# Kernel tuning notes

Hardware: AMD Instinct MI355X
Metric: run time of the kernel (lower is better)

Reference implementation:

```python
import jax, jax.numpy as jnp
import numpy as np

D = 768
B, T = 4, 4096


def _layernorm(x, gamma, bias):
    # Faithful to the (buggy) original: (x - mu/sqrt(var)) * gamma + bias,
    # with torch's default unbiased variance (ddof=1).
    mu = jnp.mean(x, axis=-1, keepdims=True)
    var = jnp.var(x, axis=-1, keepdims=True, ddof=1)
    return (x - mu / jnp.sqrt(var)) * gamma + bias


def setup_inputs() -> dict:
    key = jax.random.key(0)
    ks = jax.random.split(key, 8)
    # kaiming_uniform_ default: bound = sqrt(6 / fan_in) with a=sqrt(5) -> gain = sqrt(2/(1+5)) = sqrt(1/3)
    # bound = gain * sqrt(3/fan_in) = sqrt(1/fan_in)
    bound_attn = 1.0 / np.sqrt(D)
    bound_lin = 1.0 / np.sqrt(D)  # torch Linear default init bound
    return {
        "x": jax.random.normal(ks[0], (B, T, D), dtype=jnp.float32),
        "ln1_g": jnp.ones((D,), jnp.float32),
        "ln1_b": jnp.zeros((D,), jnp.float32),
        "wq": jax.random.uniform(ks[1], (D, D), jnp.float32, -bound_attn, bound_attn),
        "wk": jax.random.uniform(ks[2], (D, D), jnp.float32, -bound_attn, bound_attn),
        "wv": jax.random.uniform(ks[3], (D, D), jnp.float32, -bound_attn, bound_attn),
        "ln2_g": jnp.ones((D,), jnp.float32),
        "ln2_b": jnp.zeros((D,), jnp.float32),
        "fc1_w": jax.random.uniform(ks[4], (D, D), jnp.float32, -bound_lin, bound_lin),
        "fc1_b": jax.random.uniform(ks[5], (D,), jnp.float32, -bound_lin, bound_lin),
        "fc2_w": jax.random.uniform(ks[6], (D, D), jnp.float32, -bound_lin, bound_lin),
        "fc2_b": jax.random.uniform(ks[7], (D,), jnp.float32, -bound_lin, bound_lin),
    }


def reference(x, ln1_g, ln1_b, wq, wk, wv, ln2_g, ln2_b, fc1_w, fc1_b, fc2_w, fc2_b):
    d_model = x.shape[-1]
    # LN 1
    y = _layernorm(x, ln1_g, ln1_b)
    # Naive single-head attention (no causal mask, scale 1/sqrt(d_model))
    q = jnp.einsum("btk,kd->btd", y, wq)
    k = jnp.einsum("btk,kd->btd", y, wk)
    v = jnp.einsum("btk,kd->btd", y, wv)
    scale = 1.0 / jnp.sqrt(jnp.asarray(d_model, y.dtype))
    a = jax.nn.softmax(jnp.einsum("bqd,bkd->bqk", q, k) * scale, axis=-1)
    y = jnp.einsum("bqt,btd->bqd", a, v)
    # LN 2
    y = _layernorm(y, ln2_g, ln2_b)
    # MLP: Linear -> ReLU -> Linear (Dropout in eval mode = identity)
    h = jax.nn.relu(jnp.einsum("btd,od->bto", y, fc1_w) + fc1_b)
    y = jnp.einsum("btd,od->bto", h, fc2_w) + fc2_b
    # Residual
    return x + y
```

## Files before the change

kernel.cpp:

```cpp
#include <hip/hip_runtime.h>
#include <hip/hip_bf16.h>


#define DDIM 768
#define TT   4096
#define NB   4
#define ROWS (NB * TT)

using bf16 = __hip_bfloat16;
typedef __bf16 bf16x8 __attribute__((ext_vector_type(8)));
typedef float  f32x4  __attribute__((ext_vector_type(4)));
typedef unsigned short us4 __attribute__((ext_vector_type(4)));

__device__ __forceinline__ float to_f(float x) { return x; }
__device__ __forceinline__ float to_f(bf16 x) { return __bfloat162float(x); }

__device__ __forceinline__ unsigned short bfb(float f) {
  bf16 b = __float2bfloat16(f);
  return __builtin_bit_cast(unsigned short, b);
}

__device__ __forceinline__ void gload16(const void* g, void* l) {
#if __has_builtin(__builtin_amdgcn_global_load_lds)
  __builtin_amdgcn_global_load_lds(
      (const __attribute__((address_space(1))) void*)g,
      (__attribute__((address_space(3))) void*)l, 16, 0, 0);
#else
  int lane = threadIdx.x & 63;
  ((int4*)l)[lane] = *(const int4*)g;
#endif
}

template <int MODE, int SWZ, int NT, int MT>
__global__ __launch_bounds__(256) void gemm_bt(
    const bf16* __restrict__ A, int lda, long sA,
    const bf16* __restrict__ B, int ldb, long sB,
    void* __restrict__ Cout, int ldc, long sC, int K, float scale,
    const float* __restrict__ bias, const float* __restrict__ resid,
    float* __restrict__ Lsum) {
  __shared__ __align__(16) bf16 As[128 * 64];
  __shared__ __align__(16) bf16 Bs[128 * 64];
  __shared__ float Lred[128];

  int bx, by, bz;
  if constexpr (SWZ == 1) {
    const int h   = blockIdx.x;
    const int xcd = h & 7;
    const int s   = h >> 3;
    bx = s % NT;
    const int g = (s / NT) * 8 + xcd;
    by = g % MT;
    bz = g / MT;
  } else if constexpr (SWZ == 2) {
    const int h   = blockIdx.x;
    const int xcd = h & 7;
    const int s   = h >> 3;
    by = s % MT;
    const int g = (s / MT) * 8 + xcd;
    bx = g % NT;
    bz = g / NT;
  } else {
    bx = blockIdx.x; by = blockIdx.y; bz = blockIdx.z;
  }

  A += (long)bz * sA;
  B += (long)bz * sB;

  const int tid  = threadIdx.x;
  const int wave = tid >> 6;
  const int lane = tid & 63;
  const int l16  = lane & 15;
  const int lq   = lane >> 4;
  const int wm   = wave >> 1;
  const int wn   = wave & 1;
  const long tileM = (long)by * 128;
  const long tileN = (long)bx * 128;

  if constexpr (MODE == 5) {
    if (tid < 128) Lred[tid] = 0.f;
  }

  f32x4 acc[4][4] = {};

  unsigned int aoff[4], boff[4];
#pragma unroll
  for (int q = 0; q < 4; ++q) {
    const int p    = (q * 4 + wave) * 1024 + lane * 16;
    const int lg   = p ^ (((p >> 7) & 7) << 4);
    const int row  = lg >> 7;
    const int colb = lg & 127;
    aoff[q] = (unsigned int)((tileM + row) * (long)lda * 2 + colb);
    boff[q] = (unsigned int)((tileN + row) * (long)ldb * 2 + colb);
  }

  const char* Ab = (const char*)A;
  const char* Bb = (const char*)B;
  char* AsB = (char*)As;
  char* BsB = (char*)Bs;
  const int sw = (l16 & 7) << 4;

  for (int kb = 0; kb < K * 2; kb += 128) {
#pragma unroll
    for (int q = 0; q < 4; ++q)
      gload16(Ab + (aoff[q] + kb), AsB + (q * 4 + wave) * 1024);
#pragma unroll
    for (int q = 0; q < 4; ++q)
      gload16(Bb + (boff[q] + kb), BsB + (q * 4 + wave) * 1024);
    __syncthreads();

#pragma unroll
    for (int kk = 0; kk < 2; ++kk) {
      bf16x8 af[4], bf_[4];
      const int ks = (kk * 64 + lq * 16) ^ sw;
#pragma unroll
      for (int i = 0; i < 4; ++i)
        af[i] = *(const bf16x8*)(AsB + (wm * 64 + i * 16 + l16) * 128 + ks);
#pragma unroll
      for (int j = 0; j < 4; ++j)
        bf_[j] = *(const bf16x8*)(BsB + (wn * 64 + j * 16 + l16) * 128 + ks);
#pragma unroll
      for (int i = 0; i < 4; ++i)
#pragma unroll
        for (int j = 0; j < 4; ++j)
          acc[i][j] = __builtin_amdgcn_mfma_f32_16x16x32_bf16(af[i], bf_[j],
                                                              acc[i][j], 0, 0, 0);
    }
    __syncthreads();
  }

  const long base_m = tileM + wm * 64;
  const long base_n = tileN + wn * 64;

  if constexpr (MODE == 5) {
    bf16* P = (bf16*)Cout + (long)bz * sC;
    float ps[4] = {0.f, 0.f, 0.f, 0.f};
#pragma unroll
    for (int j = 0; j < 4; ++j) {
      const long colq = base_n + j * 16 + l16;
#pragma unroll
      for (int i = 0; i < 4; ++i) {
        const long krow = base_m + i * 16 + lq * 4;
        const float p0 = exp2f(acc[i][j][0] * scale);
        const float p1 = exp2f(acc[i][j][1] * scale);
        const float p2 = exp2f(acc[i][j][2] * scale);
        const float p3 = exp2f(acc[i][j][3] * scale);
        ps[j] += (p0 + p1) + (p2 + p3);
        us4 w = {bfb(p0), bfb(p1), bfb(p2), bfb(p3)};
        *(us4*)(P + colq * (long)ldc + krow) = w;
      }
    }
#pragma unroll
    for (int j = 0; j < 4; ++j) {
      float v = ps[j];
      v += __shfl_xor(v, 16);
      v += __shfl_xor(v, 32);
      if (lq == 0) atomicAdd(&Lred[wn * 64 + j * 16 + l16], v);
    }
    __syncthreads();
    if (tid < 128) atomicAdd(&Lsum[(long)bz * TT + tileN + tid], Lred[tid]);
  } else if constexpr (MODE == 6) {
    bf16* Op = (bf16*)Cout + (long)bz * sC;
    float inv[4];
#pragma unroll
    for (int j = 0; j < 4; ++j)
      inv[j] = 1.0f / Lsum[(long)bz * TT + base_n + j * 16 + l16];
#pragma unroll
    for (int j = 0; j < 4; ++j) {
      const long colq = base_n + j * 16 + l16;
#pragma unroll
      for (int i = 0; i < 4; ++i) {
        const long drow = base_m + i * 16 + lq * 4;
        us4 w = {bfb(acc[i][j][0] * inv[j]), bfb(acc[i][j][1] * inv[j]),
                 bfb(acc[i][j][2] * inv[j]), bfb(acc[i][j][3] * inv[j])};
        *(us4*)(Op + colq * (long)ldc + drow) = w;
      }
    }
  } else if constexpr (MODE == 3) {
    bf16* Hp = (bf16*)Cout;
#pragma unroll
    for (int i = 0; i < 4; ++i) {
      const long drow = base_m + i * 16 + lq * 4;
      const f32x4 bv = *(const f32x4*)&bias[drow];
#pragma unroll
      for (int j = 0; j < 4; ++j) {
        const long colt = base_n + j * 16 + l16;
        float v0 = acc[i][j][0] + bv[0]; v0 = v0 > 0.f ? v0 : 0.f;
        float v1 = acc[i][j][1] + bv[1]; v1 = v1 > 0.f ? v1 : 0.f;
        float v2 = acc[i][j][2] + bv[2]; v2 = v2 > 0.f ? v2 : 0.f;
        float v3 = acc[i][j][3] + bv[3]; v3 = v3 > 0.f ? v3 : 0.f;
        us4 w = {bfb(v0), bfb(v1), bfb(v2), bfb(v3)};
        *(us4*)(Hp + colt * (long)ldc + drow) = w;
      }
    }
  } else {
    float* Op = (float*)Cout;
#pragma unroll
    for (int i = 0; i < 4; ++i) {
      const long drow = base_m + i * 16 + lq * 4;
      const f32x4 bv = *(const f32x4*)&bias[drow];
#pragma unroll
      for (int j = 0; j < 4; ++j) {
        const long off = (base_n + j * 16 + l16) * (long)ldc + drow;
        const f32x4 rs = *(const f32x4*)&resid[off];
        f32x4 o;
        o[0] = acc[i][j][0] + bv[0] + rs[0];
        o[1] = acc[i][j][1] + bv[1] + rs[1];
        o[2] = acc[i][j][2] + bv[2] + rs[2];
        o[3] = acc[i][j][3] + bv[3] + rs[3];
        __builtin_nontemporal_store(o, (f32x4*)(Op + off));
      }
    }
  }
}

__global__ __launch_bounds__(256) void gemm_qkv(
    const bf16* __restrict__ Y,
    const bf16* __restrict__ Wq, const bf16* __restrict__ Wk,
    const bf16* __restrict__ Wv, bf16* __restrict__ Qm,
    bf16* __restrict__ Km, bf16* __restrict__ Vt) {
  __shared__ __align__(16) bf16 As[128 * 64];
  __shared__ __align__(16) bf16 Bs[128 * 64];

  const int z = blockIdx.z;
  const bf16* Ap = (z == 2) ? Wv : Y;
  const bf16* Bp = (z == 0) ? Wq : (z == 1) ? Wk : Y;

  const int tid  = threadIdx.x;
  const int wave = tid >> 6;
  const int lane = tid & 63;
  const int l16  = lane & 15;
  const int lq   = lane >> 4;
  const int wm   = wave >> 1;
  const int wn   = wave & 1;
  const long tileM = (z == 2) ? (long)blockIdx.x * 128 : (long)blockIdx.y * 128;
  const long tileN = (z == 2) ? (long)blockIdx.y * 128 : (long)blockIdx.x * 128;

  unsigned int aoff[4], boff[4];
#pragma unroll
  for (int q = 0; q < 4; ++q) {
    const int p    = (q * 4 + wave) * 1024 + lane * 16;
    const int lg   = p ^ (((p >> 7) & 7) << 4);
    const int row  = lg >> 7;
    const int colb = lg & 127;
    aoff[q] = (unsigned int)((tileM + row) * (long)DDIM * 2 + colb);
    boff[q] = (unsigned int)((tileN + row) * (long)DDIM * 2 + colb);
  }

  f32x4 acc[4][4] = {};

  const char* Ab = (const char*)Ap;
  const char* Bb = (const char*)Bp;
  char* AsB = (char*)As;
  char* BsB = (char*)Bs;
  const int sw = (l16 & 7) << 4;

  for (int kb = 0; kb < DDIM * 2; kb += 128) {
#pragma unroll
    for (int q = 0; q < 4; ++q)
      gload16(Ab + (aoff[q] + kb), AsB + (q * 4 + wave) * 1024);
#pragma unroll
    for (int q = 0; q < 4; ++q)
      gload16(Bb + (boff[q] + kb), BsB + (q * 4 + wave) * 1024);
    __syncthreads();

#pragma unroll
    for (int kk = 0; kk < 2; ++kk) {
      bf16x8 af[4], bf_[4];
      const int ks = (kk * 64 + lq * 16) ^ sw;
#pragma unroll
      for (int i = 0; i < 4; ++i)
        af[i] = *(const bf16x8*)(AsB + (wm * 64 + i * 16 + l16) * 128 + ks);
#pragma unroll
      for (int j = 0; j < 4; ++j)
        bf_[j] = *(const bf16x8*)(BsB + (wn * 64 + j * 16 + l16) * 128 + ks);
#pragma unroll
      for (int i = 0; i < 4; ++i)
#pragma unroll
        for (int j = 0; j < 4; ++j)
          acc[i][j] = __builtin_amdgcn_mfma_f32_16x16x32_bf16(af[i], bf_[j],
                                                              acc[i][j], 0, 0, 0);
    }
    __syncthreads();
  }

  const long base_m = tileM + wm * 64;
  const long base_n = tileN + wn * 64;
  bf16* Cp = (z == 0) ? Qm : (z == 1) ? Km : Vt;
  const long ldo = (z < 2) ? (long)DDIM : (long)ROWS;
#pragma unroll
  for (int i = 0; i < 4; ++i)
#pragma unroll
    for (int j = 0; j < 4; ++j)
#pragma unroll
      for (int r = 0; r < 4; ++r) {
        const long row = base_m + i * 16 + lq * 4 + r;
        const long col = base_n + j * 16 + l16;
        Cp[row * ldo + col] = __float2bfloat16(acc[i][j][r]);
      }
}

template <typename T>
__global__ __launch_bounds__(256) void ln_kernel(
    const T* __restrict__ in, const float* __restrict__ g,
    const float* __restrict__ beta, bf16* __restrict__ out,
    float* __restrict__ Lzero) {
  const long row = blockIdx.x;
  if (Lzero != nullptr && threadIdx.x == 0) Lzero[row] = 0.f;
  const T* xr = in + row * DDIM;
  const int t = threadIdx.x;
  float v0 = to_f(xr[t]), v1 = to_f(xr[t + 256]), v2 = to_f(xr[t + 512]);
  float s = v0 + v1 + v2;
  float q = v0 * v0 + v1 * v1 + v2 * v2;
#pragma unroll
  for (int o = 32; o; o >>= 1) {
    s += __shfl_down(s, o);
    q += __shfl_down(q, o);
  }
  __shared__ float sb[4], qb[4];
  if ((t & 63) == 0) { sb[t >> 6] = s; qb[t >> 6] = q; }
  __syncthreads();
  const float S = sb[0] + sb[1] + sb[2] + sb[3];
  const float Q = qb[0] + qb[1] + qb[2] + qb[3];
  const float mu  = S * (1.0f / 768.0f);
  const float var = (Q - 768.0f * mu * mu) * (1.0f / 767.0f);
  const float sub = mu / sqrtf(var);
  bf16* orow = out + row * DDIM;
  orow[t]       = __float2bfloat16((v0 - sub) * g[t]       + beta[t]);
  orow[t + 256] = __float2bfloat16((v1 - sub) * g[t + 256] + beta[t + 256]);
  orow[t + 512] = __float2bfloat16((v2 - sub) * g[t + 512] + beta[t + 512]);
}

__global__ void prep_weights(const float* __restrict__ wq,
                             const float* __restrict__ wk,
                             const float* __restrict__ wv,
                             const float* __restrict__ f1,
                             const float* __restrict__ f2,
                             bf16* wqt, bf16* wkt, bf16* wvt, bf16* f1b,
                             bf16* f2b) {
  __shared__ float tile[32][33];
  const float* src;
  bf16* dst;
  bool tr = true;
  switch (blockIdx.z) {
    case 0: src = wq; dst = wqt; break;
    case 1: src = wk; dst = wkt; break;
    case 2: src = wv; dst = wvt; break;
    case 3: src = f1; dst = f1b; tr = false; break;
    default: src = f2; dst = f2b; tr = false; break;
  }
  const int tx = threadIdx.x, ty = threadIdx.y;
  const int x = blockIdx.x * 32 + tx;
  const int y = blockIdx.y * 32 + ty;
  if (tr) {
#pragma unroll
    for (int r = 0; r < 4; ++r) tile[ty + 8 * r][tx] = src[(y + 8 * r) * DDIM + x];
    __syncthreads();
    const int ox = blockIdx.y * 32 + tx;
    const int oy = blockIdx.x * 32 + ty;
#pragma unroll
    for (int r = 0; r < 4; ++r)
      dst[(oy + 8 * r) * DDIM + ox] = __float2bfloat16(tile[tx][ty + 8 * r]);
  } else {
#pragma unroll
    for (int r = 0; r < 4; ++r)
      dst[(y + 8 * r) * DDIM + x] = __float2bfloat16(src[(y + 8 * r) * DDIM + x]);
  }
}

extern "C" void kernel_launch(void* const* d_in, const int* in_sizes, int n_in,
                              void* d_out, int out_size, void* d_ws,
                              size_t ws_size, hipStream_t stream) {
  const float* x     = (const float*)d_in[0];
  const float* ln1_g = (const float*)d_in[1];
  const float* ln1_b = (const float*)d_in[2];
  const float* wq    = (const float*)d_in[3];
  const float* wk    = (const float*)d_in[4];
  const float* wv    = (const float*)d_in[5];
  const float* ln2_g = (const float*)d_in[6];
  const float* ln2_b = (const float*)d_in[7];
  const float* f1w   = (const float*)d_in[8];
  const float* f1bias= (const float*)d_in[9];
  const float* f2w   = (const float*)d_in[10];
  const float* f2bias= (const float*)d_in[11];
  float* out = (float*)d_out;

  char* ws = (char*)d_ws;
  size_t off = 0;
  auto take = [&](size_t bytes) -> char* {
    char* p = ws + off;
    off += (bytes + 255) & ~(size_t)255;
    return p;
  };
  const size_t WB = (size_t)DDIM * DDIM * sizeof(bf16);
  const size_t MB = (size_t)ROWS * DDIM * sizeof(bf16);
  bf16* wqt = (bf16*)take(WB);
  bf16* wkt = (bf16*)take(WB);
  bf16* wvt = (bf16*)take(WB);
  bf16* f1b = (bf16*)take(WB);
  bf16* f2b = (bf16*)take(WB);
  float* Lsum = (float*)take((size_t)ROWS * sizeof(float));
  bf16* y1  = (bf16*)take(MB);
  bf16* Qm  = (bf16*)take(MB);
  bf16* Km  = (bf16*)take(MB);
  bf16* Vt  = (bf16*)take(MB);
  bf16* Sb  = (bf16*)take((size_t)NB * TT * TT * sizeof(bf16));
  bf16* O  = y1;
  bf16* y2 = Qm;
  bf16* h  = Km;

  prep_weights<<<dim3(24, 24, 5), dim3(32, 8), 0, stream>>>(
      wq, wk, wv, f1w, f2w, wqt, wkt, wvt, f1b, f2b);

  ln_kernel<float><<<ROWS, 256, 0, stream>>>(x, ln1_g, ln1_b, y1, Lsum);

  gemm_qkv<<<dim3(6, 128, 3), 256, 0, stream>>>(y1, wqt, wkt, wvt, Qm, Km, Vt);

  const float scale2 = 0.03608439182435161f * 1.4426950408889634f;
  gemm_bt<5, 1, 32, 32><<<dim3(32 * 32 * NB), 256, 0, stream>>>(
      Km, DDIM, (long)TT * DDIM, Qm, DDIM, (long)TT * DDIM, Sb, TT,
      (long)TT * TT, DDIM, scale2, nullptr, nullptr, Lsum);

  gemm_bt<6, 2, 32, 6><<<dim3(6 * 32 * NB), 256, 0, stream>>>(
      Vt, ROWS, (long)TT, Sb, TT, (long)TT * TT, O, DDIM, (long)TT * DDIM, TT,
      1.f, nullptr, nullptr, Lsum);

  ln_kernel<bf16><<<ROWS, 256, 0, stream>>>(O, ln2_g, ln2_b, y2, nullptr);

  gemm_bt<3, 2, 128, 6><<<dim3(128 * 6), 256, 0, stream>>>(
      f1b, DDIM, 0, y2, DDIM, 0, h, DDIM, 0, DDIM, 1.f, f1bias, nullptr,
      nullptr);
  gemm_bt<4, 2, 128, 6><<<dim3(128 * 6), 256, 0, stream>>>(
      f2b, DDIM, 0, h, DDIM, 0, out, DDIM, 0, DDIM, 1.f, f2bias, x, nullptr);
}
```

Before: 590.8 us.

## Split-K the attention PV GEMM and fold softmax normalization into LN2

The PV GEMM now splits its 4096-long reduction into two halves run as separate blocks, each writing an unnormalized bf16 partial output to its own buffer. The second LayerNorm kernel sums the two partials and divides by the softmax row sum before normalizing. This is meant to raise parallelism and occupancy in the PV stage and remove the per-element division there. In exchange it adds an extra partial buffer write and read, and some precision loss from storing partials in bf16.

```diff
diff --git a/kernel.cpp b/kernel.cpp
--- a/kernel.cpp
+++ b/kernel.cpp
@@ -63,8 +63,11 @@
     bx = blockIdx.x; by = blockIdx.y; bz = blockIdx.z;
   }
 
-  A += (long)bz * sA;
-  B += (long)bz * sB;
+  int kz = 0;
+  if constexpr (MODE == 7) { kz = bz >> 2; bz &= 3; }
+
+  A += (long)bz * sA + (long)kz * 2048;
+  B += (long)bz * sB + (long)kz * 2048;
 
   const int tid  = threadIdx.x;
   const int wave = tid >> 6;
@@ -158,20 +161,16 @@
     }
     __syncthreads();
     if (tid < 128) atomicAdd(&Lsum[(long)bz * TT + tileN + tid], Lred[tid]);
-  } else if constexpr (MODE == 6) {
-    bf16* Op = (bf16*)Cout + (long)bz * sC;
-    float inv[4];
-#pragma unroll
-    for (int j = 0; j < 4; ++j)
-      inv[j] = 1.0f / Lsum[(long)bz * TT + base_n + j * 16 + l16];
+  } else if constexpr (MODE == 7) {
+    bf16* Op = (bf16*)Cout + (long)kz * ((long)ROWS * DDIM) + (long)bz * sC;
 #pragma unroll
     for (int j = 0; j < 4; ++j) {
       const long colq = base_n + j * 16 + l16;
 #pragma unroll
       for (int i = 0; i < 4; ++i) {
         const long drow = base_m + i * 16 + lq * 4;
-        us4 w = {bfb(acc[i][j][0] * inv[j]), bfb(acc[i][j][1] * inv[j]),
-                 bfb(acc[i][j][2] * inv[j]), bfb(acc[i][j][3] * inv[j])};
+        us4 w = {bfb(acc[i][j][0]), bfb(acc[i][j][1]),
+                 bfb(acc[i][j][2]), bfb(acc[i][j][3])};
         *(us4*)(Op + colq * (long)ldc + drow) = w;
       }
     }
@@ -299,9 +298,10 @@
       }
 }
 
-template <typename T>
+template <typename T, int DUAL>
 __global__ __launch_bounds__(256) void ln_kernel(
-    const T* __restrict__ in, const float* __restrict__ g,
+    const T* __restrict__ in, const T* __restrict__ in2,
+    const float* __restrict__ Ldiv, const float* __restrict__ g,
     const float* __restrict__ beta, bf16* __restrict__ out,
     float* __restrict__ Lzero) {
   const long row = blockIdx.x;
@@ -309,6 +309,12 @@
   const T* xr = in + row * DDIM;
   const int t = threadIdx.x;
   float v0 = to_f(xr[t]), v1 = to_f(xr[t + 256]), v2 = to_f(xr[t + 512]);
+  if constexpr (DUAL) {
+    const T* xr2 = in2 + row * DDIM;
+    v0 += to_f(xr2[t]); v1 += to_f(xr2[t + 256]); v2 += to_f(xr2[t + 512]);
+    const float invL = 1.0f / Ldiv[row];
+    v0 *= invL; v1 *= invL; v2 *= invL;
+  }
   float s = v0 + v1 + v2;
   float q = v0 * v0 + v1 * v1 + v2 * v2;
 #pragma unroll
@@ -404,14 +410,16 @@
   bf16* Km  = (bf16*)take(MB);
   bf16* Vt  = (bf16*)take(MB);
   bf16* Sb  = (bf16*)take((size_t)NB * TT * TT * sizeof(bf16));
-  bf16* O  = y1;
-  bf16* y2 = Qm;
-  bf16* h  = Km;
+  bf16* O0 = y1;
+  bf16* O1 = Qm;
+  bf16* y2 = Km;
+  bf16* h  = y1;
 
   prep_weights<<<dim3(24, 24, 5), dim3(32, 8), 0, stream>>>(
       wq, wk, wv, f1w, f2w, wqt, wkt, wvt, f1b, f2b);
 
-  ln_kernel<float><<<ROWS, 256, 0, stream>>>(x, ln1_g, ln1_b, y1, Lsum);
+  ln_kernel<float, 0><<<ROWS, 256, 0, stream>>>(x, nullptr, nullptr, ln1_g,
+                                                ln1_b, y1, Lsum);
 
   gemm_qkv<<<dim3(6, 128, 3), 256, 0, stream>>>(y1, wqt, wkt, wvt, Qm, Km, Vt);
 
@@ -420,11 +428,12 @@
       Km, DDIM, (long)TT * DDIM, Qm, DDIM, (long)TT * DDIM, Sb, TT,
       (long)TT * TT, DDIM, scale2, nullptr, nullptr, Lsum);
 
-  gemm_bt<6, 2, 32, 6><<<dim3(6 * 32 * NB), 256, 0, stream>>>(
-      Vt, ROWS, (long)TT, Sb, TT, (long)TT * TT, O, DDIM, (long)TT * DDIM, TT,
-      1.f, nullptr, nullptr, Lsum);
-
-  ln_kernel<bf16><<<ROWS, 256, 0, stream>>>(O, ln2_g, ln2_b, y2, nullptr);
+  gemm_bt<7, 2, 32, 6><<<dim3(6 * 32 * NB * 2), 256, 0, stream>>>(
+      Vt, ROWS, (long)TT, Sb, TT, (long)TT * TT, O0, DDIM, (long)TT * DDIM,
+      TT / 2, 1.f, nullptr, nullptr, nullptr);
+
+  ln_kernel<bf16, 1><<<ROWS, 256, 0, stream>>>(O0, O1, Lsum, ln2_g, ln2_b, y2,
+                                               nullptr);
 
   gemm_bt<3, 2, 128, 6><<<dim3(128 * 6), 256, 0, stream>>>(
       f1b, DDIM, 0, y2, DDIM, 0, h, DDIM, 0, DDIM, 1.f, f1bias, nullptr,
```

New measurement: 566.9 us. 1.04x faster.

## Add dedicated 64x128-tile P·V GEMM kernel to double block count

Applied to the files above, without the earlier changes.

Replaces the generic 128x128 gemm_bt mode 6 used for the P·V product with a specialized kernel using 64x128 tiles (each wave computes 32x64), giving 1536 blocks instead of 768. The finer grid is meant to improve CU occupancy and load balance on the long-K (4096) attention-value GEMM. Smaller tiles lower arithmetic intensity per block and mean more re-reads of the large S matrix from memory. The unused MODE 6 path and the non-swizzled grid fallback are removed from gemm_bt.

```diff
diff --git a/kernel.cpp b/kernel.cpp
--- a/kernel.cpp
+++ b/kernel.cpp
@@ -51,7 +51,7 @@
     const int g = (s / NT) * 8 + xcd;
     by = g % MT;
     bz = g / MT;
-  } else if constexpr (SWZ == 2) {
+  } else {
     const int h   = blockIdx.x;
     const int xcd = h & 7;
     const int s   = h >> 3;
@@ -59,8 +59,6 @@
     const int g = (s / MT) * 8 + xcd;
     bx = g % NT;
     bz = g / NT;
-  } else {
-    bx = blockIdx.x; by = blockIdx.y; bz = blockIdx.z;
   }
 
   A += (long)bz * sA;
@@ -158,23 +156,6 @@
     }
     __syncthreads();
     if (tid < 128) atomicAdd(&Lsum[(long)bz * TT + tileN + tid], Lred[tid]);
-  } else if constexpr (MODE == 6) {
-    bf16* Op = (bf16*)Cout + (long)bz * sC;
-    float inv[4];
-#pragma unroll
-    for (int j = 0; j < 4; ++j)
-      inv[j] = 1.0f / Lsum[(long)bz * TT + base_n + j * 16 + l16];
-#pragma unroll
-    for (int j = 0; j < 4; ++j) {
-      const long colq = base_n + j * 16 + l16;
-#pragma unroll
-      for (int i = 0; i < 4; ++i) {
-        const long drow = base_m + i * 16 + lq * 4;
-        us4 w = {bfb(acc[i][j][0] * inv[j]), bfb(acc[i][j][1] * inv[j]),
-                 bfb(acc[i][j][2] * inv[j]), bfb(acc[i][j][3] * inv[j])};
-        *(us4*)(Op + colq * (long)ldc + drow) = w;
-      }
-    }
   } else if constexpr (MODE == 3) {
     bf16* Hp = (bf16*)Cout;
 #pragma unroll
@@ -209,6 +190,100 @@
         o[3] = acc[i][j][3] + bv[3] + rs[3];
         __builtin_nontemporal_store(o, (f32x4*)(Op + off));
       }
+    }
+  }
+}
+
+__global__ __launch_bounds__(256) void gemm_pv(
+    const bf16* __restrict__ A, const bf16* __restrict__ B,
+    bf16* __restrict__ O, const float* __restrict__ Lsum) {
+  __shared__ __align__(16) bf16 S[(64 + 128) * 64];
+
+  const int h   = blockIdx.x;
+  const int xcd = h & 7;
+  const int s   = h >> 3;
+  const int by  = s % 12;
+  const int g   = (s / 12) * 8 + xcd;
+  const int bx  = g % 32;
+  const int bz  = g / 32;
+
+  const char* Ab = (const char*)(A + (long)bz * TT);
+  const char* Bb = (const char*)(B + (long)bz * (long)TT * TT);
+
+  const int tid  = threadIdx.x;
+  const int wave = tid >> 6;
+  const int lane = tid & 63;
+  const int l16  = lane & 15;
+  const int lq   = lane >> 4;
+  const int wm   = wave >> 1;
+  const int wn   = wave & 1;
+  const long tileM = (long)by * 64;
+  const long tileN = (long)bx * 128;
+
+  const char* gsrc[6];
+  int ldsoff[6];
+#pragma unroll
+  for (int u = 0; u < 6; ++u) {
+    const int c = wave + 4 * u;
+    ldsoff[u] = c * 1024;
+    if (c < 8) {
+      const int p    = c * 1024 + lane * 16;
+      const int row  = p >> 7;
+      const int colb = (p & 127) ^ ((row & 7) << 4);
+      gsrc[u] = Ab + (tileM + row) * (long)ROWS * 2 + colb;
+    } else {
+      const int p    = (c - 8) * 1024 + lane * 16;
+      const int row  = p >> 7;
+      const int colb = (p & 127) ^ ((row & 7) << 4);
+      gsrc[u] = Bb + (tileN + row) * (long)TT * 2 + colb;
+    }
+  }
+
+  f32x4 acc[2][4] = {};
+  char* Sb_ = (char*)S;
+  const int sw = (l16 & 7) << 4;
+
+  for (long kb = 0; kb < (long)TT * 2; kb += 128) {
+#pragma unroll
+    for (int u = 0; u < 6; ++u)
+      gload16(gsrc[u] + kb, Sb_ + ldsoff[u]);
+    __syncthreads();
+
+#pragma unroll
+    for (int kk = 0; kk < 2; ++kk) {
+      bf16x8 af[2], bf_[4];
+      const int ks = (kk * 64 + lq * 16) ^ sw;
+#pragma unroll
+      for (int i = 0; i < 2; ++i)
+        af[i] = *(const bf16x8*)(Sb_ + (wm * 32 + i * 16 + l16) * 128 + ks);
+#pragma unroll
+      for (int j = 0; j < 4; ++j)
+        bf_[j] = *(const bf16x8*)(Sb_ + 8192 +
+                                  (wn * 64 + j * 16 + l16) * 128 + ks);
+#pragma unroll
+      for (int i = 0; i < 2; ++i)
+#pragma unroll
+        for (int j = 0; j < 4; ++j)
+          acc[i][j] = __builtin_amdgcn_mfma_f32_16x16x32_bf16(af[i], bf_[j],
+                                                              acc[i][j], 0, 0, 0);
+    }
+    __syncthreads();
+  }
+
+  bf16* Op = O + (long)bz * (long)TT * DDIM;
+  float inv[4];
+#pragma unroll
+  for (int j = 0; j < 4; ++j)
+    inv[j] = 1.0f / Lsum[(long)bz * TT + tileN + wn * 64 + j * 16 + l16];
+#pragma unroll
+  for (int j = 0; j < 4; ++j) {
+    const long colq = tileN + wn * 64 + j * 16 + l16;
+#pragma unroll
+    for (int i = 0; i < 2; ++i) {
+      const long drow = tileM + wm * 32 + i * 16 + lq * 4;
+      us4 w = {bfb(acc[i][j][0] * inv[j]), bfb(acc[i][j][1] * inv[j]),
+               bfb(acc[i][j][2] * inv[j]), bfb(acc[i][j][3] * inv[j])};
+      *(us4*)(Op + colq * (long)DDIM + drow) = w;
     }
   }
 }
@@ -420,9 +495,7 @@
       Km, DDIM, (long)TT * DDIM, Qm, DDIM, (long)TT * DDIM, Sb, TT,
       (long)TT * TT, DDIM, scale2, nullptr, nullptr, Lsum);
 
-  gemm_bt<6, 2, 32, 6><<<dim3(6 * 32 * NB), 256, 0, stream>>>(
-      Vt, ROWS, (long)TT, Sb, TT, (long)TT * TT, O, DDIM, (long)TT * DDIM, TT,
-      1.f, nullptr, nullptr, Lsum);
+  gemm_pv<<<dim3(12 * 32 * NB), 256, 0, stream>>>(Vt, Sb, O, Lsum);
 
   ln_kernel<bf16><<<ROWS, 256, 0, stream>>>(O, ln2_g, ln2_b, y2, nullptr);
 
```

Measured after the change: 587.5 us. No clear change (-0.6%).
